# Performance work log

Measured on AMD Instinct MI355X. Metric: run time of the kernel, lower is better.

The kernel has to match this reference:

```python
import jax, jax.numpy as jnp
import numpy as np
import math

D_MODEL = 1024
NHEADS = 16
HEAD_DIM = D_MODEL // NHEADS


def make_pe(n, d):
    # sinusoidal positional encoding table, shape [n, d]
    pos = jnp.arange(n, dtype=jnp.float32)[:, None]
    div = jnp.exp(jnp.arange(0, d, 2, dtype=jnp.float32) * (-math.log(10000.0) / d))
    pe = jnp.zeros((n, d), dtype=jnp.float32)
    pe = pe.at[:, 0::2].set(jnp.sin(pos * div))
    pe = pe.at[:, 1::2].set(jnp.cos(pos * div))
    return pe


def setup_inputs() -> dict:
    key = jax.random.key(0)
    ks = jax.random.split(key, 6)
    B, S, D = 2, 2048, D_MODEL
    x = jax.random.normal(ks[0], (B, S, D), dtype=jnp.float32)
    mask = jax.random.randint(ks[1], (1, 1, S, S), 0, 2, dtype=jnp.int32)
    qkv_w = jax.random.normal(ks[2], (3 * D, D), dtype=jnp.float32) * (1.0 / math.sqrt(D))
    qkv_b = jax.random.normal(ks[3], (3 * D,), dtype=jnp.float32) * 0.02
    fc_w = jax.random.normal(ks[4], (D, D), dtype=jnp.float32) * (1.0 / math.sqrt(D))
    fc_b = jax.random.normal(ks[5], (D,), dtype=jnp.float32) * 0.02
    return {"x": x, "mask": mask, "qkv_w": qkv_w, "qkv_b": qkv_b, "fc_w": fc_w, "fc_b": fc_b}


def reference(x, mask, qkv_w, qkv_b, fc_w, fc_b):
    B, S, D = x.shape
    H, Hd = NHEADS, HEAD_DIM
    qkv = jnp.einsum('bsd,ed->bse', x, qkv_w) + qkv_b  # [B,S,3D]
    xq, xk, xv = jnp.split(qkv, 3, axis=-1)
    # Faithful to source: pe[:x.size(0)] slices batch_size rows, broadcast over seq dim
    pe = make_pe(B, D)[:, None, :]  # [B,1,D]
    xq = xq + pe
    xk = xk + pe
    # [B,S,D] -> [B,H,S,Hd]
    xq = xq.reshape(B, S, H, Hd).transpose(0, 2, 1, 3)
    xk = xk.reshape(B, S, H, Hd).transpose(0, 2, 1, 3)
    xv = xv.reshape(B, S, H, Hd).transpose(0, 2, 1, 3)
    scores = jnp.einsum('bhqd,bhkd->bhqk', xq, xk) / math.sqrt(Hd)
    scores = jnp.where(mask == 1, jnp.float32(-1e9), scores)
    probs = jax.nn.softmax(scores, axis=-1)
    out = jnp.einsum('bhqk,bhkd->bhqd', probs, xv)
    out = out.transpose(0, 2, 1, 3).reshape(B, S, D)
    return jnp.einsum('bsd,ed->bse', out, fc_w) + fc_b
```

## Files before the change

kernel.cpp:

```cpp
#include <hip/hip_runtime.h>
#include <hip/hip_bf16.h>
#include <cstdint>

typedef __attribute__((ext_vector_type(8))) short short8;
typedef __attribute__((ext_vector_type(4))) float f32x4;
typedef __attribute__((ext_vector_type(16))) float f32x16;
typedef __attribute__((ext_vector_type(4))) unsigned uint4v;

#define DEV static __device__ __forceinline__

DEV f32x4 mfma16(short8 a, short8 b, f32x4 c) {
    return __builtin_amdgcn_mfma_f32_16x16x32_bf16(a, b, c, 0, 0, 0);
}
DEV f32x16 mfma32(short8 a, short8 b, f32x16 c) {
    return __builtin_amdgcn_mfma_f32_32x32x16_bf16(a, b, c, 0, 0, 0);
}

DEV unsigned short f2bf(float f) {
    __hip_bfloat16 h = __float2bfloat16(f);
    return __builtin_bit_cast(unsigned short, h);
}

DEV unsigned cvtpk(float lo, float hi) {
    unsigned r;
    asm("v_cvt_pk_bf16_f32 %0, %1, %2" : "=v"(r) : "v"(lo), "v"(hi));
    return r;
}
DEV void plswap(unsigned& a, unsigned& b) {
    asm volatile("v_permlane32_swap_b32 %0, %1" : "+v"(a), "+v"(b));
}

#define GLOAD16(gp, lp)                                                        \
    __builtin_amdgcn_global_load_lds(                                          \
        (const __attribute__((address_space(1))) unsigned int*)(uintptr_t)(gp),\
        (__attribute__((address_space(3))) unsigned int*)(uintptr_t)(lp),      \
        16, 0, 0)


__global__ void pe_kernel(float* __restrict__ pe) {
    int i = threadIdx.x;
    if (i >= 512) return;
    float div = expf((float)(2 * i) * (-9.210340371976184f / 1024.0f));
    pe[2 * i]          = 0.0f;
    pe[2 * i + 1]      = 1.0f;
    pe[1024 + 2 * i]     = sinf(div);
    pe[1024 + 2 * i + 1] = cosf(div);
}

__global__ void cvt3(const float* __restrict__ x, const float* __restrict__ wq,
                     const float* __restrict__ wf, unsigned short* __restrict__ xb,
                     unsigned short* __restrict__ wqb, unsigned short* __restrict__ wfb) {
    int i = blockIdx.x * blockDim.x + threadIdx.x;
    const float* src; unsigned short* dst; int off;
    if (i < 1048576)      { src = x;  dst = xb;  off = i; }
    else if (i < 1835008) { src = wq; dst = wqb; off = i - 1048576; }
    else                  { src = wf; dst = wfb; off = i - 1835008; }
    float4 v = ((const float4*)src)[off];
    ushort4 o;
    o.x = f2bf(v.x); o.y = f2bf(v.y); o.z = f2bf(v.z); o.w = f2bf(v.w);
    ((ushort4*)dst)[off] = o;
}

__global__ void pack_mask(const int* __restrict__ mask, unsigned int* __restrict__ wT) {
    int o = blockIdx.x * blockDim.x + threadIdx.x;
    int kb = o >> 11, row = o & 2047;
    const int4* m4 = (const int4*)(mask + (size_t)row * 2048 + kb * 32);
    unsigned int bits = 0;
#pragma unroll
    for (int j = 0; j < 8; j++) {
        int4 v = m4[j];
        bits |= (unsigned)(v.x & 1) << (4 * j);
        bits |= (unsigned)(v.y & 1) << (4 * j + 1);
        bits |= (unsigned)(v.z & 1) << (4 * j + 2);
        bits |= (unsigned)(v.w & 1) << (4 * j + 3);
    }
    wT[o] = bits;
}

DEV void gemm_mainloop(const unsigned short* __restrict__ A,
                       const unsigned short* __restrict__ Bm,
                       int m0, int n0, f32x4 (&acc)[4][4],
                       unsigned short* As, unsigned short* Bs) {
    const int t = threadIdx.x;
    const int w = t >> 6;
    const int l = t & 63, lr = l & 15, lg = l >> 4;
    const int wr = w >> 1, wc = w & 1;
    const int srow = t >> 2;
    const int scg = ((t & 3) ^ ((t >> 3) & 3)) * 8;
#pragma unroll
    for (int i = 0; i < 4; i++)
#pragma unroll
        for (int j = 0; j < 4; j++) acc[i][j] = f32x4{0.f, 0.f, 0.f, 0.f};

    const unsigned short* Ap = A + (size_t)(m0 + srow) * 1024 + scg;
    const unsigned short* Bp = Bm + (size_t)(n0 + srow) * 1024 + scg;
    unsigned short* dA = As + w * 512;
    unsigned short* dB = Bs + w * 512;

    const int slot = (lg ^ ((lr >> 1) & 3)) * 8;
    const unsigned short* Ar = As + (wr * 64 + lr) * 32 + slot;
    const unsigned short* Br = Bs + (wc * 64 + lr) * 32 + slot;

#define STAGE(buf, k0)                                                \
    {                                                                 \
        GLOAD16(Ap + (k0), dA + (buf) * 4096);                        \
        GLOAD16(Ap + 64 * 1024 + (k0), dA + (buf) * 4096 + 2048);     \
        GLOAD16(Bp + (k0), dB + (buf) * 4096);                        \
        GLOAD16(Bp + 64 * 1024 + (k0), dB + (buf) * 4096 + 2048);     \
    }

    STAGE(0, 0);
#pragma unroll 2
    for (int k0 = 0; k0 < 1024; k0 += 32) {
        const int cur = (k0 >> 5) & 1;
        __syncthreads();
        if (k0 + 32 < 1024) STAGE(cur ^ 1, k0 + 32);
        short8 af[4], bfr[4];
#pragma unroll
        for (int i = 0; i < 4; i++)
            af[i] = *(const short8*)(Ar + cur * 4096 + i * 512);
#pragma unroll
        for (int j = 0; j < 4; j++)
            bfr[j] = *(const short8*)(Br + cur * 4096 + j * 512);
#pragma unroll
        for (int i = 0; i < 4; i++)
#pragma unroll
            for (int j = 0; j < 4; j++)
                acc[i][j] = mfma16(af[i], bfr[j], acc[i][j]);
    }
#undef STAGE
}

__global__ __launch_bounds__(256) void qkv_gemm(
    const unsigned short* __restrict__ x, const unsigned short* __restrict__ wq,
    const float* __restrict__ bias, const float* __restrict__ pe,
    unsigned short* __restrict__ qo, unsigned short* __restrict__ ko,
    unsigned short* __restrict__ vt) {
    __shared__ unsigned short As[2 * 4096], Bs[2 * 4096];
    const int m0 = blockIdx.y * 128, n0 = blockIdx.x * 128;
    f32x4 acc[4][4];
    gemm_mainloop(x, wq, m0, n0, acc, As, Bs);

    const int t = threadIdx.x, w = t >> 6, l = t & 63;
    const int wr = w >> 1, wc = w & 1, lr = l & 15, lg = l >> 4;
#pragma unroll
    for (int i = 0; i < 4; i++) {
#pragma unroll
        for (int j = 0; j < 4; j++) {
            const int n = n0 + wc * 64 + j * 16 + lr;
            const int part = n >> 10, d = n & 1023, h = d >> 6, hd = d & 63;
            const float bia = bias[n];
#pragma unroll
            for (int r = 0; r < 4; r++) {
                const int m = m0 + wr * 64 + i * 16 + lg * 4 + r;
                const int b = m >> 11, s = m & 2047;
                const int bh = b * 16 + h;
                float v = acc[i][j][r] + bia;
                if (part == 2) {
                    const size_t off = (size_t)bh * 131072 + (s >> 5) * 2048 +
                                       (hd >> 5) * 1024 + ((s >> 4) & 1) * 512 +
                                       (((s >> 3) & 1) * 32 + (hd & 31)) * 8 + (s & 7);
                    vt[off] = f2bf(v);
                } else {
                    const size_t off = (size_t)bh * 131072 + (s >> 5) * 2048 +
                                       (hd >> 4) * 512 +
                                       (((hd >> 3) & 1) * 32 + (s & 31)) * 8 + (hd & 7);
                    if (part == 0) {
                        v = (v + pe[b * 1024 + d]) * 0.1803368801111204f;
                        qo[off] = f2bf(v);
                    } else {
                        v += pe[b * 1024 + d];
                        ko[off] = f2bf(v);
                    }
                }
            }
        }
    }
}

__global__ __launch_bounds__(256) void fc_gemm(
    const unsigned short* __restrict__ a, const unsigned short* __restrict__ wf,
    const float* __restrict__ bias, float* __restrict__ out) {
    __shared__ unsigned short As[2 * 4096], Bs[2 * 4096];
    const int m0 = blockIdx.y * 128, n0 = blockIdx.x * 128;
    f32x4 acc[4][4];
    gemm_mainloop(a, wf, m0, n0, acc, As, Bs);

    const int t = threadIdx.x, w = t >> 6, l = t & 63;
    const int wr = w >> 1, wc = w & 1, lr = l & 15, lg = l >> 4;
#pragma unroll
    for (int i = 0; i < 4; i++) {
#pragma unroll
        for (int j = 0; j < 4; j++) {
            const int n = n0 + wc * 64 + j * 16 + lr;
            const float bia = bias[n];
#pragma unroll
            for (int r = 0; r < 4; r++) {
                const int m = m0 + wr * 64 + i * 16 + lg * 4 + r;
                out[(size_t)m * 1024 + n] = acc[i][j][r] + bia;
            }
        }
    }
}

__global__ __launch_bounds__(256) void attn(
    const unsigned short* __restrict__ q, const unsigned short* __restrict__ k,
    const unsigned short* __restrict__ vt, const unsigned int* __restrict__ mw,
    float* __restrict__ po, float* __restrict__ ms) {
    const int t = threadIdx.x, w = t >> 6;
    const int l = t & 63, c = l & 31, hi = l >> 5;
    const int bid = blockIdx.x;
    const int xcd = bid & 7, idx = bid >> 3;
    const int bh = xcd * 4 + (idx & 3);
    const int rest = idx >> 2;
    const int chunk = rest & 1, qg = rest >> 1;
    const int qb = qg * 4 + w;
    const int q0 = qb * 32;
    const int tile = bh * 64 + qb;
    const int kb0 = chunk * 32;

    const unsigned short* qfb = q + (size_t)bh * 131072 + qb * 2048 + l * 8;
    const unsigned short* kfb = k + (size_t)bh * 131072 + l * 8;
    const unsigned short* vfb = vt + (size_t)bh * 131072 + l * 8;

    short8 qf[4];
#pragma unroll
    for (int d = 0; d < 4; d++)
        qf[d] = *(const short8*)(qfb + d * 512);

    short8 ones;
#pragma unroll
    for (int i = 0; i < 8; i++) ones[i] = (short)0x3F80;

    short8 kf[4], vf[2][2];
#pragma unroll
    for (int d = 0; d < 4; d++) kf[d] = *(const short8*)(kfb + kb0 * 2048 + d * 512);
#pragma unroll
    for (int kc = 0; kc < 2; kc++) {
        vf[0][kc] = *(const short8*)(vfb + kb0 * 2048 + kc * 512);
        vf[1][kc] = *(const short8*)(vfb + kb0 * 2048 + 1024 + kc * 512);
    }
    unsigned int wd = mw[kb0 * 2048 + q0 + c];

    f32x16 OT0, OT1, LS;
#pragma unroll
    for (int i = 0; i < 16; i++) { OT0[i] = 0.f; OT1[i] = 0.f; LS[i] = 0.f; }

#pragma unroll 2
    for (int kb = kb0; kb < kb0 + 32; kb++) {
        f32x16 S;
#pragma unroll
        for (int i = 0; i < 16; i++) S[i] = 0.f;
#pragma unroll
        for (int d = 0; d < 4; d++) S = mfma32(kf[d], qf[d], S);

        short8 kn[4], vn[2][2];
        const unsigned short* kpn = kfb + (kb + 1) * 2048;
        const unsigned short* vpn = vfb + (kb + 1) * 2048;
#pragma unroll
        for (int d = 0; d < 4; d++) kn[d] = *(const short8*)(kpn + d * 512);
#pragma unroll
        for (int kc = 0; kc < 2; kc++) {
            vn[0][kc] = *(const short8*)(vpn + kc * 512);
            vn[1][kc] = *(const short8*)(vpn + 1024 + kc * 512);
        }
        const unsigned int wn = mw[(kb + 1) * 2048 + q0 + c];

        const unsigned int wds = wd >> (4 * hi);
        float p[16];
#pragma unroll
        for (int g = 0; g < 4; g++)
#pragma unroll
            for (int u = 0; u < 4; u++)
                p[g * 4 + u] = (wds & (1u << (8 * g + u))) ? -1e9f : S[g * 4 + u];
#pragma unroll
        for (int i = 0; i < 16; i++) p[i] = exp2f(p[i]);

        unsigned w8[8];
#pragma unroll
        for (int g = 0; g < 4; g++) {
            w8[2 * g]     = cvtpk(p[4 * g], p[4 * g + 1]);
            w8[2 * g + 1] = cvtpk(p[4 * g + 2], p[4 * g + 3]);
        }
        short8 pa[2];
#pragma unroll
        for (int kc = 0; kc < 2; kc++) {
            unsigned a0 = w8[4 * kc], a2 = w8[4 * kc + 2];
            plswap(a0, a2);
            unsigned a1 = w8[4 * kc + 1], a3 = w8[4 * kc + 3];
            plswap(a1, a3);
            uint4v tv; tv[0] = a0; tv[1] = a1; tv[2] = a2; tv[3] = a3;
            pa[kc] = __builtin_bit_cast(short8, tv);
        }

        OT0 = mfma32(vf[0][0], pa[0], OT0);
        OT0 = mfma32(vf[0][1], pa[1], OT0);
        OT1 = mfma32(vf[1][0], pa[0], OT1);
        OT1 = mfma32(vf[1][1], pa[1], OT1);
        LS  = mfma32(ones,     pa[0], LS);
        LS  = mfma32(ones,     pa[1], LS);

#pragma unroll
        for (int d = 0; d < 4; d++) kf[d] = kn[d];
#pragma unroll
        for (int kc = 0; kc < 2; kc++) { vf[0][kc] = vn[0][kc]; vf[1][kc] = vn[1][kc]; }
        wd = wn;
    }

    if (hi == 0)
        ms[((size_t)tile * 2 + chunk) * 32 + c] = LS[0];
    float* pb = po + ((size_t)tile * 2 + chunk) * 2048;
#pragma unroll
    for (int i = 0; i < 16; i++) {
        const int kr = (i & 3) + 8 * (i >> 2) + 4 * hi;
        pb[kr * 32 + c]        = OT0[i];
        pb[(32 + kr) * 32 + c] = OT1[i];
    }
}

__global__ __launch_bounds__(256) void combine(
    const float* __restrict__ po, const float* __restrict__ ms,
    unsigned short* __restrict__ ao) {
    const int cid = blockIdx.x * 4 + (threadIdx.x >> 6);
    const int bh = cid >> 6, qb = cid & 63;
    const int b = bh >> 4, h = bh & 15, q0 = qb * 32;
    const int l = threadIdx.x & 63, q = l >> 1, dh = (l & 1) * 32;

    const float L = ms[(size_t)cid * 64 + q] + ms[(size_t)cid * 64 + 32 + q];
    const float inv = 1.0f / L;

    const float* pb = po + (size_t)cid * 2 * 2048;
    unsigned short* gout = ao + ((size_t)(b * 2048 + q0 + q)) * 1024 + h * 64 + dh;
#pragma unroll
    for (int ch = 0; ch < 4; ch++) {
        uint4v pk;
#pragma unroll
        for (int u = 0; u < 4; u++) {
            const int j0 = ch * 8 + 2 * u;
            float a0 = pb[(dh + j0) * 32 + q]     + pb[2048 + (dh + j0) * 32 + q];
            float a1 = pb[(dh + j0 + 1) * 32 + q] + pb[2048 + (dh + j0 + 1) * 32 + q];
            pk[u] = cvtpk(a0 * inv, a1 * inv);
        }
        *(uint4v*)(gout + ch * 8) = pk;
    }
}

extern "C" void kernel_launch(void* const* d_in, const int* in_sizes, int n_in,
                              void* d_out, int out_size, void* d_ws, size_t ws_size,
                              hipStream_t stream) {
    const float* x     = (const float*)d_in[0];
    const int*   mask  = (const int*)d_in[1];
    const float* qkv_w = (const float*)d_in[2];
    const float* qkv_b = (const float*)d_in[3];
    const float* fc_w  = (const float*)d_in[4];
    const float* fc_b  = (const float*)d_in[5];
    float* out = (float*)d_out;

    char* ws = (char*)d_ws;
    size_t off = 0;
    auto alloc = [&](size_t bytes) {
        off = (off + 255) & ~(size_t)255;
        void* p = ws + off;
        off += bytes;
        return p;
    };
    float*          pe     = (float*)alloc(2 * 1024 * 4);
    unsigned int*   mwords = (unsigned int*)alloc((size_t)2048 * 64 * 4);
    unsigned short* xb     = (unsigned short*)alloc((size_t)4096 * 1024 * 2);
    unsigned short* wqkv   = (unsigned short*)alloc((size_t)3072 * 1024 * 2);
    unsigned short* wfc    = (unsigned short*)alloc((size_t)1024 * 1024 * 2);
    unsigned short* qb16   = (unsigned short*)alloc((size_t)2 * 16 * 2048 * 64 * 2);
    unsigned short* kb16   = (unsigned short*)alloc((size_t)2 * 16 * 2048 * 64 * 2);
    unsigned short* vtb    = (unsigned short*)alloc((size_t)2 * 16 * 64 * 2048 * 2);
    unsigned short* attn_o = (unsigned short*)alloc((size_t)4096 * 1024 * 2);
    float*          po     = (float*)alloc((size_t)2048 * 2 * 2048 * 4);
    float*          msb    = (float*)alloc((size_t)2048 * 2 * 32 * 4);

    pe_kernel<<<1, 512, 0, stream>>>(pe);
    cvt3<<<8192, 256, 0, stream>>>(x, qkv_w, fc_w, xb, wqkv, wfc);
    pack_mask<<<512, 256, 0, stream>>>(mask, mwords);
    qkv_gemm<<<dim3(24, 32), 256, 0, stream>>>(xb, wqkv, qkv_b, pe, qb16, kb16, vtb);
    attn<<<dim3(1024), 256, 0, stream>>>(qb16, kb16, vtb, mwords, po, msb);
    combine<<<dim3(512), 256, 0, stream>>>(po, msb, attn_o);
    fc_gemm<<<dim3(8, 32), 256, 0, stream>>>(attn_o, wfc, fc_b, out);
}
```

Measured before the change: 169.5 us.

## Process two query tiles per wave to reuse K/V loads; compute row sums with VALU

Each wave in the attention kernel now handles two 32-row query tiles (qb and qb+32), so every K and V fragment loaded from global memory feeds two QK^T and two PV MFMA chains. The grid is halved to match. The softmax denominator now comes from a VALU reduction plus a cross-half shuffle instead of extra MFMAs against a vector of ones, and S starts from a zero register kept opaque to the compiler. In exchange, register pressure and per-wave serial work rise, and occupancy drops because there are half as many blocks.

```diff
diff --git a/kernel.cpp b/kernel.cpp
--- a/kernel.cpp
+++ b/kernel.cpp
@@ -214,23 +214,26 @@
     const int bh = xcd * 4 + (idx & 3);
     const int rest = idx >> 2;
     const int chunk = rest & 1, qg = rest >> 1;
-    const int qb = qg * 4 + w;
-    const int q0 = qb * 32;
-    const int tile = bh * 64 + qb;
+    const int qbA = qg * 4 + w;
+    const int qbB = qbA + 32;
     const int kb0 = chunk * 32;
 
-    const unsigned short* qfb = q + (size_t)bh * 131072 + qb * 2048 + l * 8;
-    const unsigned short* kfb = k + (size_t)bh * 131072 + l * 8;
-    const unsigned short* vfb = vt + (size_t)bh * 131072 + l * 8;
-
-    short8 qf[4];
-#pragma unroll
-    for (int d = 0; d < 4; d++)
-        qf[d] = *(const short8*)(qfb + d * 512);
-
-    short8 ones;
-#pragma unroll
-    for (int i = 0; i < 8; i++) ones[i] = (short)0x3F80;
+    const unsigned short* qfbA = q + (size_t)bh * 131072 + qbA * 2048 + l * 8;
+    const unsigned short* kfb  = k + (size_t)bh * 131072 + l * 8;
+    const unsigned short* vfb  = vt + (size_t)bh * 131072 + l * 8;
+
+    short8 qfA[4], qfB[4];
+#pragma unroll
+    for (int d = 0; d < 4; d++) {
+        qfA[d] = *(const short8*)(qfbA + d * 512);
+        qfB[d] = *(const short8*)(qfbA + 65536 + d * 512);
+    }
+
+    float z = 0.f;
+    asm volatile("" : "+v"(z));
+    f32x16 FZ;
+#pragma unroll
+    for (int i = 0; i < 16; i++) FZ[i] = z;
 
     short8 kf[4], vf[2][2];
 #pragma unroll
@@ -240,19 +243,19 @@
         vf[0][kc] = *(const short8*)(vfb + kb0 * 2048 + kc * 512);
         vf[1][kc] = *(const short8*)(vfb + kb0 * 2048 + 1024 + kc * 512);
     }
-    unsigned int wd = mw[kb0 * 2048 + q0 + c];
-
-    f32x16 OT0, OT1, LS;
-#pragma unroll
-    for (int i = 0; i < 16; i++) { OT0[i] = 0.f; OT1[i] = 0.f; LS[i] = 0.f; }
+    unsigned wdA = mw[kb0 * 2048 + qbA * 32 + c];
+    unsigned wdB = mw[kb0 * 2048 + qbB * 32 + c];
+
+    f32x16 OA0, OA1, OB0, OB1;
+#pragma unroll
+    for (int i = 0; i < 16; i++) { OA0[i] = 0.f; OA1[i] = 0.f; OB0[i] = 0.f; OB1[i] = 0.f; }
+    float lA = 0.f, lB = 0.f;
 
 #pragma unroll 2
     for (int kb = kb0; kb < kb0 + 32; kb++) {
-        f32x16 S;
-#pragma unroll
-        for (int i = 0; i < 16; i++) S[i] = 0.f;
-#pragma unroll
-        for (int d = 0; d < 4; d++) S = mfma32(kf[d], qf[d], S);
+        f32x16 SA = mfma32(kf[0], qfA[0], FZ);
+#pragma unroll
+        for (int d = 1; d < 4; d++) SA = mfma32(kf[d], qfA[d], SA);
 
         short8 kn[4], vn[2][2];
         const unsigned short* kpn = kfb + (kb + 1) * 2048;
@@ -264,57 +267,106 @@
             vn[0][kc] = *(const short8*)(vpn + kc * 512);
             vn[1][kc] = *(const short8*)(vpn + 1024 + kc * 512);
         }
-        const unsigned int wn = mw[(kb + 1) * 2048 + q0 + c];
-
-        const unsigned int wds = wd >> (4 * hi);
-        float p[16];
-#pragma unroll
-        for (int g = 0; g < 4; g++)
-#pragma unroll
-            for (int u = 0; u < 4; u++)
-                p[g * 4 + u] = (wds & (1u << (8 * g + u))) ? -1e9f : S[g * 4 + u];
-#pragma unroll
-        for (int i = 0; i < 16; i++) p[i] = exp2f(p[i]);
-
-        unsigned w8[8];
-#pragma unroll
-        for (int g = 0; g < 4; g++) {
-            w8[2 * g]     = cvtpk(p[4 * g], p[4 * g + 1]);
-            w8[2 * g + 1] = cvtpk(p[4 * g + 2], p[4 * g + 3]);
-        }
-        short8 pa[2];
-#pragma unroll
-        for (int kc = 0; kc < 2; kc++) {
-            unsigned a0 = w8[4 * kc], a2 = w8[4 * kc + 2];
-            plswap(a0, a2);
-            unsigned a1 = w8[4 * kc + 1], a3 = w8[4 * kc + 3];
-            plswap(a1, a3);
-            uint4v tv; tv[0] = a0; tv[1] = a1; tv[2] = a2; tv[3] = a3;
-            pa[kc] = __builtin_bit_cast(short8, tv);
-        }
-
-        OT0 = mfma32(vf[0][0], pa[0], OT0);
-        OT0 = mfma32(vf[0][1], pa[1], OT0);
-        OT1 = mfma32(vf[1][0], pa[0], OT1);
-        OT1 = mfma32(vf[1][1], pa[1], OT1);
-        LS  = mfma32(ones,     pa[0], LS);
-        LS  = mfma32(ones,     pa[1], LS);
+        const unsigned wnA = mw[(kb + 1) * 2048 + qbA * 32 + c];
+        const unsigned wnB = mw[(kb + 1) * 2048 + qbB * 32 + c];
+
+        {
+            const unsigned wds = wdA >> (4 * hi);
+            float p[16];
+#pragma unroll
+            for (int g = 0; g < 4; g++)
+#pragma unroll
+                for (int u = 0; u < 4; u++)
+                    p[g * 4 + u] = (wds & (1u << (8 * g + u))) ? -1e9f : SA[g * 4 + u];
+#pragma unroll
+            for (int i = 0; i < 16; i++) p[i] = exp2f(p[i]);
+            float rs = (((p[0] + p[1]) + (p[2] + p[3])) + ((p[4] + p[5]) + (p[6] + p[7]))) +
+                       (((p[8] + p[9]) + (p[10] + p[11])) + ((p[12] + p[13]) + (p[14] + p[15])));
+            rs += __shfl_xor(rs, 32);
+            lA += rs;
+            unsigned w8[8];
+#pragma unroll
+            for (int g = 0; g < 4; g++) {
+                w8[2 * g]     = cvtpk(p[4 * g], p[4 * g + 1]);
+                w8[2 * g + 1] = cvtpk(p[4 * g + 2], p[4 * g + 3]);
+            }
+            short8 pa[2];
+#pragma unroll
+            for (int kc = 0; kc < 2; kc++) {
+                unsigned a0 = w8[4 * kc], a2 = w8[4 * kc + 2];
+                plswap(a0, a2);
+                unsigned a1 = w8[4 * kc + 1], a3 = w8[4 * kc + 3];
+                plswap(a1, a3);
+                uint4v tv; tv[0] = a0; tv[1] = a1; tv[2] = a2; tv[3] = a3;
+                pa[kc] = __builtin_bit_cast(short8, tv);
+            }
+            OA0 = mfma32(vf[0][0], pa[0], OA0);
+            OA0 = mfma32(vf[0][1], pa[1], OA0);
+            OA1 = mfma32(vf[1][0], pa[0], OA1);
+            OA1 = mfma32(vf[1][1], pa[1], OA1);
+        }
+
+        f32x16 SB = mfma32(kf[0], qfB[0], FZ);
+#pragma unroll
+        for (int d = 1; d < 4; d++) SB = mfma32(kf[d], qfB[d], SB);
+
+        {
+            const unsigned wds = wdB >> (4 * hi);
+            float p[16];
+#pragma unroll
+            for (int g = 0; g < 4; g++)
+#pragma unroll
+                for (int u = 0; u < 4; u++)
+                    p[g * 4 + u] = (wds & (1u << (8 * g + u))) ? -1e9f : SB[g * 4 + u];
+#pragma unroll
+            for (int i = 0; i < 16; i++) p[i] = exp2f(p[i]);
+            float rs = (((p[0] + p[1]) + (p[2] + p[3])) + ((p[4] + p[5]) + (p[6] + p[7]))) +
+                       (((p[8] + p[9]) + (p[10] + p[11])) + ((p[12] + p[13]) + (p[14] + p[15])));
+            rs += __shfl_xor(rs, 32);
+            lB += rs;
+            unsigned w8[8];
+#pragma unroll
+            for (int g = 0; g < 4; g++) {
+                w8[2 * g]     = cvtpk(p[4 * g], p[4 * g + 1]);
+                w8[2 * g + 1] = cvtpk(p[4 * g + 2], p[4 * g + 3]);
+            }
+            short8 pa[2];
+#pragma unroll
+            for (int kc = 0; kc < 2; kc++) {
+                unsigned a0 = w8[4 * kc], a2 = w8[4 * kc + 2];
+                plswap(a0, a2);
+                unsigned a1 = w8[4 * kc + 1], a3 = w8[4 * kc + 3];
+                plswap(a1, a3);
+                uint4v tv; tv[0] = a0; tv[1] = a1; tv[2] = a2; tv[3] = a3;
+                pa[kc] = __builtin_bit_cast(short8, tv);
+            }
+            OB0 = mfma32(vf[0][0], pa[0], OB0);
+            OB0 = mfma32(vf[0][1], pa[1], OB0);
+            OB1 = mfma32(vf[1][0], pa[0], OB1);
+            OB1 = mfma32(vf[1][1], pa[1], OB1);
+        }
 
 #pragma unroll
         for (int d = 0; d < 4; d++) kf[d] = kn[d];
 #pragma unroll
         for (int kc = 0; kc < 2; kc++) { vf[0][kc] = vn[0][kc]; vf[1][kc] = vn[1][kc]; }
-        wd = wn;
-    }
-
-    if (hi == 0)
-        ms[((size_t)tile * 2 + chunk) * 32 + c] = LS[0];
-    float* pb = po + ((size_t)tile * 2 + chunk) * 2048;
+        wdA = wnA; wdB = wnB;
+    }
+
+    const int tileA = bh * 64 + qbA, tileB = bh * 64 + qbB;
+    if (hi == 0) {
+        ms[((size_t)tileA * 2 + chunk) * 32 + c] = lA;
+        ms[((size_t)tileB * 2 + chunk) * 32 + c] = lB;
+    }
+    float* pbA = po + ((size_t)tileA * 2 + chunk) * 2048;
+    float* pbB = po + ((size_t)tileB * 2 + chunk) * 2048;
 #pragma unroll
     for (int i = 0; i < 16; i++) {
         const int kr = (i & 3) + 8 * (i >> 2) + 4 * hi;
-        pb[kr * 32 + c]        = OT0[i];
-        pb[(32 + kr) * 32 + c] = OT1[i];
+        pbA[kr * 32 + c]        = OA0[i];
+        pbA[(32 + kr) * 32 + c] = OA1[i];
+        pbB[kr * 32 + c]        = OB0[i];
+        pbB[(32 + kr) * 32 + c] = OB1[i];
     }
 }
 
@@ -380,7 +432,7 @@
     cvt3<<<8192, 256, 0, stream>>>(x, qkv_w, fc_w, xb, wqkv, wfc);
     pack_mask<<<512, 256, 0, stream>>>(mask, mwords);
     qkv_gemm<<<dim3(24, 32), 256, 0, stream>>>(xb, wqkv, qkv_b, pe, qb16, kb16, vtb);
-    attn<<<dim3(1024), 256, 0, stream>>>(qb16, kb16, vtb, mwords, po, msb);
+    attn<<<dim3(512), 256, 0, stream>>>(qb16, kb16, vtb, mwords, po, msb);
     combine<<<dim3(512), 256, 0, stream>>>(po, msb, attn_o);
     fc_gemm<<<dim3(8, 32), 256, 0, stream>>>(attn_o, wfc, fc_b, out);
 }
```

Result: slower. 180.5 us (+6.5%).

## Fuse split-K attention combine into attn kernel via shared memory

Applied to the files above, without the earlier changes.

Remaps attention blocks so each block's four waves cover two query tiles with both key chunks, then reduces the partial outputs and row sums through LDS and writes normalized bf16 output directly. This removes the separate combine kernel and the fp32 partial-output round trip through global memory. It also seeds the score MFMA chain from an opaque zero vector instead of re-zeroing per iteration. The cost is about 33 KB of shared memory per block, which may limit occupancy, plus a block-wide barrier.

```diff
diff --git a/kernel.cpp b/kernel.cpp
--- a/kernel.cpp
+++ b/kernel.cpp
@@ -206,17 +206,17 @@
 __global__ __launch_bounds__(256) void attn(
     const unsigned short* __restrict__ q, const unsigned short* __restrict__ k,
     const unsigned short* __restrict__ vt, const unsigned int* __restrict__ mw,
-    float* __restrict__ po, float* __restrict__ ms) {
+    unsigned short* __restrict__ ao) {
+    __shared__ float CL[4][2080];
     const int t = threadIdx.x, w = t >> 6;
     const int l = t & 63, c = l & 31, hi = l >> 5;
     const int bid = blockIdx.x;
     const int xcd = bid & 7, idx = bid >> 3;
     const int bh = xcd * 4 + (idx & 3);
-    const int rest = idx >> 2;
-    const int chunk = rest & 1, qg = rest >> 1;
-    const int qb = qg * 4 + w;
-    const int q0 = qb * 32;
-    const int tile = bh * 64 + qb;
+    const int qpair = idx >> 2;
+    const int chunk = w & 1;
+    const int qb = qpair * 2 + (w >> 1);
+    const int b = bh >> 4, h = bh & 15;
     const int kb0 = chunk * 32;
 
     const unsigned short* qfb = q + (size_t)bh * 131072 + qb * 2048 + l * 8;
@@ -232,6 +232,12 @@
 #pragma unroll
     for (int i = 0; i < 8; i++) ones[i] = (short)0x3F80;
 
+    float z = 0.f;
+    asm volatile("" : "+v"(z));
+    f32x16 FZ;
+#pragma unroll
+    for (int i = 0; i < 16; i++) FZ[i] = z;
+
     short8 kf[4], vf[2][2];
 #pragma unroll
     for (int d = 0; d < 4; d++) kf[d] = *(const short8*)(kfb + kb0 * 2048 + d * 512);
@@ -240,7 +246,7 @@
         vf[0][kc] = *(const short8*)(vfb + kb0 * 2048 + kc * 512);
         vf[1][kc] = *(const short8*)(vfb + kb0 * 2048 + 1024 + kc * 512);
     }
-    unsigned int wd = mw[kb0 * 2048 + q0 + c];
+    unsigned int wd = mw[kb0 * 2048 + qb * 32 + c];
 
     f32x16 OT0, OT1, LS;
 #pragma unroll
@@ -248,11 +254,9 @@
 
 #pragma unroll 2
     for (int kb = kb0; kb < kb0 + 32; kb++) {
-        f32x16 S;
-#pragma unroll
-        for (int i = 0; i < 16; i++) S[i] = 0.f;
-#pragma unroll
-        for (int d = 0; d < 4; d++) S = mfma32(kf[d], qf[d], S);
+        f32x16 S = mfma32(kf[0], qf[0], FZ);
+#pragma unroll
+        for (int d = 1; d < 4; d++) S = mfma32(kf[d], qf[d], S);
 
         short8 kn[4], vn[2][2];
         const unsigned short* kpn = kfb + (kb + 1) * 2048;
@@ -264,7 +268,7 @@
             vn[0][kc] = *(const short8*)(vpn + kc * 512);
             vn[1][kc] = *(const short8*)(vpn + 1024 + kc * 512);
         }
-        const unsigned int wn = mw[(kb + 1) * 2048 + q0 + c];
+        const unsigned int wn = mw[(kb + 1) * 2048 + qb * 32 + c];
 
         const unsigned int wds = wd >> (4 * hi);
         float p[16];
@@ -307,42 +311,33 @@
         wd = wn;
     }
 
-    if (hi == 0)
-        ms[((size_t)tile * 2 + chunk) * 32 + c] = LS[0];
-    float* pb = po + ((size_t)tile * 2 + chunk) * 2048;
+    float* R = CL[w];
 #pragma unroll
     for (int i = 0; i < 16; i++) {
         const int kr = (i & 3) + 8 * (i >> 2) + 4 * hi;
-        pb[kr * 32 + c]        = OT0[i];
-        pb[(32 + kr) * 32 + c] = OT1[i];
-    }
-}
-
-__global__ __launch_bounds__(256) void combine(
-    const float* __restrict__ po, const float* __restrict__ ms,
-    unsigned short* __restrict__ ao) {
-    const int cid = blockIdx.x * 4 + (threadIdx.x >> 6);
-    const int bh = cid >> 6, qb = cid & 63;
-    const int b = bh >> 4, h = bh & 15, q0 = qb * 32;
-    const int l = threadIdx.x & 63, q = l >> 1, dh = (l & 1) * 32;
-
-    const float L = ms[(size_t)cid * 64 + q] + ms[(size_t)cid * 64 + 32 + q];
-    const float inv = 1.0f / L;
-
-    const float* pb = po + (size_t)cid * 2 * 2048;
-    unsigned short* gout = ao + ((size_t)(b * 2048 + q0 + q)) * 1024 + h * 64 + dh;
-#pragma unroll
-    for (int ch = 0; ch < 4; ch++) {
-        uint4v pk;
-#pragma unroll
-        for (int u = 0; u < 4; u++) {
-            const int j0 = ch * 8 + 2 * u;
-            float a0 = pb[(dh + j0) * 32 + q]     + pb[2048 + (dh + j0) * 32 + q];
-            float a1 = pb[(dh + j0 + 1) * 32 + q] + pb[2048 + (dh + j0 + 1) * 32 + q];
-            pk[u] = cvtpk(a0 * inv, a1 * inv);
-        }
-        *(uint4v*)(gout + ch * 8) = pk;
-    }
+        R[kr * 32 + c]        = OT0[i];
+        R[(32 + kr) * 32 + c] = OT1[i];
+    }
+    if (hi == 0) R[2048 + c] = LS[0];
+    __syncthreads();
+
+    const float* C0 = CL[(w >> 1) * 2];
+    const float* C1 = CL[(w >> 1) * 2 + 1];
+    const int qq = l >> 1, db = (l & 1) * 16 + (w & 1) * 32;
+    const float inv = 1.0f / (C0[2048 + qq] + C1[2048 + qq]);
+    const int row = b * 2048 + (qpair * 2 + (w >> 1)) * 32 + qq;
+    unsigned short* gout = ao + (size_t)row * 1024 + h * 64 + db;
+    uint4v pk0, pk1;
+#pragma unroll
+    for (int u = 0; u < 4; u++) {
+        const int d0 = db + 2 * u, d1 = db + 8 + 2 * u;
+        pk0[u] = cvtpk((C0[d0 * 32 + qq] + C1[d0 * 32 + qq]) * inv,
+                       (C0[(d0 + 1) * 32 + qq] + C1[(d0 + 1) * 32 + qq]) * inv);
+        pk1[u] = cvtpk((C0[d1 * 32 + qq] + C1[d1 * 32 + qq]) * inv,
+                       (C0[(d1 + 1) * 32 + qq] + C1[(d1 + 1) * 32 + qq]) * inv);
+    }
+    *(uint4v*)(gout)     = pk0;
+    *(uint4v*)(gout + 8) = pk1;
 }
 
 extern "C" void kernel_launch(void* const* d_in, const int* in_sizes, int n_in,
@@ -373,14 +368,11 @@
     unsigned short* kb16   = (unsigned short*)alloc((size_t)2 * 16 * 2048 * 64 * 2);
     unsigned short* vtb    = (unsigned short*)alloc((size_t)2 * 16 * 64 * 2048 * 2);
     unsigned short* attn_o = (unsigned short*)alloc((size_t)4096 * 1024 * 2);
-    float*          po     = (float*)alloc((size_t)2048 * 2 * 2048 * 4);
-    float*          msb    = (float*)alloc((size_t)2048 * 2 * 32 * 4);
 
     pe_kernel<<<1, 512, 0, stream>>>(pe);
     cvt3<<<8192, 256, 0, stream>>>(x, qkv_w, fc_w, xb, wqkv, wfc);
     pack_mask<<<512, 256, 0, stream>>>(mask, mwords);
     qkv_gemm<<<dim3(24, 32), 256, 0, stream>>>(xb, wqkv, qkv_b, pe, qb16, kb16, vtb);
-    attn<<<dim3(1024), 256, 0, stream>>>(qb16, kb16, vtb, mwords, po, msb);
-    combine<<<dim3(512), 256, 0, stream>>>(po, msb, attn_o);
+    attn<<<dim3(1024), 256, 0, stream>>>(qb16, kb16, vtb, mwords, attn_o);
     fc_gemm<<<dim3(8, 32), 256, 0, stream>>>(attn_o, wfc, fc_b, out);
 }
```

After: 164.2 us. 3.2% less time.
